# Optimization experiments

Measured on AMD Instinct MI355X. Metric: run time of the kernel, lower is better.

The kernel has to match this reference:

```python
import jax, jax.numpy as jnp
import numpy as np

N = 100000        # nodes
E = 1600000       # edges (avg degree 16)
D_NODE = 32
D_EDGE = 16
H = 64
C = 5


def setup_inputs() -> dict:
    key = jax.random.key(0)
    ks = jax.random.split(key, 11)
    x = jax.random.normal(ks[0], (N, D_NODE), jnp.float32)
    edge_index = jax.random.randint(ks[1], (2, E), 0, N, jnp.int32)
    edge_attr = jax.random.normal(ks[2], (E, D_EDGE), jnp.float32)
    W1 = jax.random.normal(ks[3], (D_NODE, H), jnp.float32) / np.sqrt(D_NODE)
    b1 = jax.random.normal(ks[4], (H,), jnp.float32) * 0.02
    W2 = jax.random.normal(ks[5], (H, H), jnp.float32) / np.sqrt(H)
    b2 = jax.random.normal(ks[6], (H,), jnp.float32) * 0.02
    Wc1 = jax.random.normal(ks[7], (2 * H + D_EDGE, 64), jnp.float32) / np.sqrt(2 * H + D_EDGE)
    bc1 = jax.random.normal(ks[8], (64,), jnp.float32) * 0.02
    Wc2 = jax.random.normal(ks[9], (64, C), jnp.float32) / np.sqrt(64)
    bc2 = jax.random.normal(ks[10], (C,), jnp.float32) * 0.02
    return {"x": x, "edge_index": edge_index, "edge_attr": edge_attr,
            "W1": W1, "b1": b1, "W2": W2, "b2": b2,
            "Wc1": Wc1, "bc1": bc1, "Wc2": Wc2, "bc2": bc2}


def gcn_conv(x, W, b, src, dst, n):
    h = x @ W                                   # [n, H]
    loop = jnp.arange(n, dtype=src.dtype)
    s = jnp.concatenate([src, loop])            # self-loops appended
    d = jnp.concatenate([dst, loop])
    deg = jax.ops.segment_sum(jnp.ones_like(s, h.dtype), d, num_segments=n)
    dinv = jax.lax.rsqrt(deg)                   # deg >= 1 due to self-loops
    norm = dinv[s] * dinv[d]                    # [E+n]
    out = jax.ops.segment_sum(h[s] * norm[:, None], d, num_segments=n)
    return out + b


def reference(x, edge_index, edge_attr, W1, b1, W2, b2, Wc1, bc1, Wc2, bc2):
    src, dst = edge_index[0], edge_index[1]
    n = x.shape[0]
    h = jax.nn.relu(gcn_conv(x, W1, b1, src, dst, n))
    h = gcn_conv(h, W2, b2, src, dst, n)
    # gather-concat edge features: [E, 2H + D_EDGE]
    ef = jnp.concatenate([h[src], h[dst], edge_attr], axis=1)
    out = jax.nn.relu(ef @ Wc1 + bc1) @ Wc2 + bc2
    return out
```

## Files before the change

kernel.cpp:

```cpp
#include <hip/hip_runtime.h>
#include <hip/hip_bf16.h>


typedef __attribute__((ext_vector_type(8))) short  bf16x8;
typedef __attribute__((ext_vector_type(16))) float f32x16;

__device__ inline short f2bf(float f)
{
    union { float f; unsigned u; } v; v.f = f;
    unsigned r = v.u + 0x7fff + ((v.u >> 16) & 1);
    return (short)(r >> 16);
}

__device__ inline float2 bfp2f(unsigned u)
{
    union { unsigned u; float f; } a, b;
    a.u = u << 16;
    b.u = u & 0xffff0000u;
    return make_float2(a.f, b.f);
}

__device__ inline unsigned packbf2(float a, float b)
{
    return (unsigned)(unsigned short)f2bf(a) | ((unsigned)(unsigned short)f2bf(b) << 16);
}

__global__ __launch_bounds__(256) void k_bcount(const int* __restrict__ ei, int* __restrict__ bcnt, int E)
{
    __shared__ int h[512];
    for (int i = threadIdx.x; i < 512; i += 256) h[i] = 0;
    __syncthreads();
    for (long e = (long)blockIdx.x * 256 + threadIdx.x; e < E; e += (long)gridDim.x * 256)
        atomicAdd(&h[ei[E + e] >> 8], 1);
    __syncthreads();
    for (int i = threadIdx.x; i < 512; i += 256)
        if (h[i]) atomicAdd(&bcnt[i], h[i]);
}

__global__ __launch_bounds__(512) void k_bscan(const int* __restrict__ bcnt, int nbk, int* __restrict__ bstart)
{
    __shared__ int s[512];
    int t = threadIdx.x;
    int v = (t < nbk) ? bcnt[t] : 0;
    s[t] = v;
    __syncthreads();
    for (int o = 1; o < 512; o <<= 1) {
        int a = (t >= o) ? s[t - o] : 0;
        __syncthreads();
        s[t] += a;
        __syncthreads();
    }
    if (t < nbk) bstart[t + 1] = s[t];
    if (t == 0) bstart[0] = 0;
}

__global__ __launch_bounds__(256) void k_binscatter(const int* __restrict__ ei, const int* __restrict__ bstart,
                                                    int* __restrict__ bcur, int2* __restrict__ ebs, int E)
{
    __shared__ int cnt[512], gb[512];
    const int tid = threadIdx.x;
    for (int i = tid; i < 512; i += 256) cnt[i] = 0;
    __syncthreads();
    const int base = blockIdx.x * 4096;
    int d[16], lp[16];
#pragma unroll
    for (int i = 0; i < 16; ++i) {
        int e = base + i * 256 + tid;
        if (e < E) {
            d[i] = ei[E + e];
            lp[i] = atomicAdd(&cnt[d[i] >> 8], 1);
        } else d[i] = -1;
    }
    __syncthreads();
    for (int i = tid; i < 512; i += 256) gb[i] = cnt[i] ? atomicAdd(&bcur[i], cnt[i]) : 0;
    __syncthreads();
#pragma unroll
    for (int i = 0; i < 16; ++i) {
        if (d[i] >= 0) {
            int e = base + i * 256 + tid;
            int b = d[i] >> 8;
            int2 p;
            p.x = ei[e];
            p.y = d[i];
            ebs[(size_t)bstart[b] + gb[b] + lp[i]] = p;
        }
    }
}

__global__ __launch_bounds__(256) void k_build(const int2* __restrict__ ebs, const int* __restrict__ bstart,
                                               int* __restrict__ rs, int* __restrict__ col,
                                               float* __restrict__ dinv,
                                               const float* __restrict__ x, unsigned short* __restrict__ xs,
                                               int N, int E)
{
    __shared__ int cnt[256], lstart[256], cnt2[256];
    const int b = blockIdx.x;
    const int base = b << 8;
    const int tid = threadIdx.x;
    cnt[tid] = 0; cnt2[tid] = 0;
    __syncthreads();
    const int s0 = bstart[b], s1 = bstart[b + 1];
    for (int i = s0 + tid; i < s1; i += 256) atomicAdd(&cnt[ebs[i].y - base], 1);
    __syncthreads();
    const int v = cnt[tid];
    lstart[tid] = v;
    __syncthreads();
    for (int o = 1; o < 256; o <<= 1) {
        int a = (tid >= o) ? lstart[tid - o] : 0;
        __syncthreads();
        lstart[tid] += a;
        __syncthreads();
    }
    const int node = base + tid;
    if (node < N) {
        rs[node] = s0 + lstart[tid] - v;
        dinv[node] = rsqrtf((float)(v + 1));
    }
    if (b == 0 && tid == 0) rs[N] = E;
    __syncthreads();
    for (int i = s0 + tid; i < s1; i += 256) {
        int2 p = ebs[i];
        int ln = p.y - base;
        int pos = atomicAdd(&cnt2[ln], 1);
        col[s0 + (lstart[ln] - cnt[ln]) + pos] = p.x;
    }
#pragma unroll
    for (int i = 0; i < 16; ++i) {
        int id = i * 256 + tid;
        int ni = id >> 4, pr = id & 15;
        int nd = base + ni;
        if (nd < N) {
            float dv = rsqrtf((float)(cnt[ni] + 1));
            float2 xv = *(const float2*)&x[(size_t)nd * 32 + pr * 2];
            *(unsigned*)(xs + (size_t)nd * 32 + pr * 2) = packbf2(xv.x * dv, xv.y * dv);
        }
    }
}

__global__ __launch_bounds__(256) void k_prep(const float* __restrict__ Wc1, const float* __restrict__ Wc2,
                                              const float* __restrict__ W2, const float* __restrict__ W1,
                                              short* __restrict__ Wc1T, short* __restrict__ Wc2T,
                                              short* __restrict__ W2T, short* __restrict__ W1T)
{
    int t = blockIdx.x * 256 + threadIdx.x;
    if (t < 9216) {
        int j = t / 144, k = t - j * 144;
        Wc1T[t] = f2bf(Wc1[k * 64 + j]);
    } else if (t < 11264) {
        int u = t - 9216;
        int rr = u / 64, p = u - rr * 64;
        int k = (p >> 1) + ((p & 1) << 5);
        Wc2T[u] = (rr < 5) ? f2bf(Wc2[k * 5 + rr]) : (short)0;
    } else if (t < 15360) {
        int u = t - 11264;
        int j = u / 64, k = u - j * 64;
        W2T[u] = f2bf(W2[k * 64 + j]);
    } else if (t < 17408) {
        int u = t - 15360;
        int j = u / 32, k = u - j * 32;
        W1T[u] = f2bf(W1[k * 64 + j]);
    }
}

__global__ __launch_bounds__(256) void k_agg_x(const unsigned short* __restrict__ xs,
                                               const float* __restrict__ dinv,
                                               const int* __restrict__ rs, const int* __restrict__ col,
                                               unsigned short* __restrict__ xagg, int n)
{
    const int tid = threadIdx.x;
    const int l   = tid & 7;
    const int v   = blockIdx.x * 32 + (tid >> 3);
    if (v >= n) return;

    uint2 sv = *(const uint2*)(xs + (size_t)v * 32 + l * 4);
    float2 aL = bfp2f(sv.x), aH = bfp2f(sv.y);
    int i = rs[v];
    const int end = rs[v + 1];
    for (; i + 8 <= end; i += 8) {
        int c0 = col[i],     c1 = col[i + 1], c2 = col[i + 2], c3 = col[i + 3];
        int c4 = col[i + 4], c5 = col[i + 5], c6 = col[i + 6], c7 = col[i + 7];
        uint2 u0 = *(const uint2*)(xs + (size_t)c0 * 32 + l * 4);
        uint2 u1 = *(const uint2*)(xs + (size_t)c1 * 32 + l * 4);
        uint2 u2 = *(const uint2*)(xs + (size_t)c2 * 32 + l * 4);
        uint2 u3 = *(const uint2*)(xs + (size_t)c3 * 32 + l * 4);
        uint2 u4 = *(const uint2*)(xs + (size_t)c4 * 32 + l * 4);
        uint2 u5 = *(const uint2*)(xs + (size_t)c5 * 32 + l * 4);
        uint2 u6 = *(const uint2*)(xs + (size_t)c6 * 32 + l * 4);
        uint2 u7 = *(const uint2*)(xs + (size_t)c7 * 32 + l * 4);
        float2 p;
        p = bfp2f(u0.x); aL.x += p.x; aL.y += p.y; p = bfp2f(u0.y); aH.x += p.x; aH.y += p.y;
        p = bfp2f(u1.x); aL.x += p.x; aL.y += p.y; p = bfp2f(u1.y); aH.x += p.x; aH.y += p.y;
        p = bfp2f(u2.x); aL.x += p.x; aL.y += p.y; p = bfp2f(u2.y); aH.x += p.x; aH.y += p.y;
        p = bfp2f(u3.x); aL.x += p.x; aL.y += p.y; p = bfp2f(u3.y); aH.x += p.x; aH.y += p.y;
        p = bfp2f(u4.x); aL.x += p.x; aL.y += p.y; p = bfp2f(u4.y); aH.x += p.x; aH.y += p.y;
        p = bfp2f(u5.x); aL.x += p.x; aL.y += p.y; p = bfp2f(u5.y); aH.x += p.x; aH.y += p.y;
        p = bfp2f(u6.x); aL.x += p.x; aL.y += p.y; p = bfp2f(u6.y); aH.x += p.x; aH.y += p.y;
        p = bfp2f(u7.x); aL.x += p.x; aL.y += p.y; p = bfp2f(u7.y); aH.x += p.x; aH.y += p.y;
    }
    for (; i < end; ++i) {
        uint2 u = *(const uint2*)(xs + (size_t)col[i] * 32 + l * 4);
        float2 p;
        p = bfp2f(u.x); aL.x += p.x; aL.y += p.y;
        p = bfp2f(u.y); aH.x += p.x; aH.y += p.y;
    }
    const float dv = dinv[v];
    uint2 o;
    o.x = packbf2(dv * aL.x, dv * aL.y);
    o.y = packbf2(dv * aH.x, dv * aH.y);
    *(uint2*)(xagg + (size_t)v * 32 + l * 4) = o;
}

__global__ __launch_bounds__(256) void k_agg64(const unsigned short* __restrict__ hsc,
                                               const float* __restrict__ dinv,
                                               const int* __restrict__ rs, const int* __restrict__ col,
                                               unsigned short* __restrict__ out, int n)
{
    const int tid = threadIdx.x;
    const int l   = tid & 15;
    const int v   = blockIdx.x * 16 + (tid >> 4);
    if (v >= n) return;

    uint2 sv = *(const uint2*)(hsc + (size_t)v * 64 + l * 4);
    float2 aL = bfp2f(sv.x), aH = bfp2f(sv.y);
    int i = rs[v];
    const int end = rs[v + 1];
    for (; i + 8 <= end; i += 8) {
        int c0 = col[i],     c1 = col[i + 1], c2 = col[i + 2], c3 = col[i + 3];
        int c4 = col[i + 4], c5 = col[i + 5], c6 = col[i + 6], c7 = col[i + 7];
        uint2 u0 = *(const uint2*)(hsc + (size_t)c0 * 64 + l * 4);
        uint2 u1 = *(const uint2*)(hsc + (size_t)c1 * 64 + l * 4);
        uint2 u2 = *(const uint2*)(hsc + (size_t)c2 * 64 + l * 4);
        uint2 u3 = *(const uint2*)(hsc + (size_t)c3 * 64 + l * 4);
        uint2 u4 = *(const uint2*)(hsc + (size_t)c4 * 64 + l * 4);
        uint2 u5 = *(const uint2*)(hsc + (size_t)c5 * 64 + l * 4);
        uint2 u6 = *(const uint2*)(hsc + (size_t)c6 * 64 + l * 4);
        uint2 u7 = *(const uint2*)(hsc + (size_t)c7 * 64 + l * 4);
        float2 p;
        p = bfp2f(u0.x); aL.x += p.x; aL.y += p.y; p = bfp2f(u0.y); aH.x += p.x; aH.y += p.y;
        p = bfp2f(u1.x); aL.x += p.x; aL.y += p.y; p = bfp2f(u1.y); aH.x += p.x; aH.y += p.y;
        p = bfp2f(u2.x); aL.x += p.x; aL.y += p.y; p = bfp2f(u2.y); aH.x += p.x; aH.y += p.y;
        p = bfp2f(u3.x); aL.x += p.x; aL.y += p.y; p = bfp2f(u3.y); aH.x += p.x; aH.y += p.y;
        p = bfp2f(u4.x); aL.x += p.x; aL.y += p.y; p = bfp2f(u4.y); aH.x += p.x; aH.y += p.y;
        p = bfp2f(u5.x); aL.x += p.x; aL.y += p.y; p = bfp2f(u5.y); aH.x += p.x; aH.y += p.y;
        p = bfp2f(u6.x); aL.x += p.x; aL.y += p.y; p = bfp2f(u6.y); aH.x += p.x; aH.y += p.y;
        p = bfp2f(u7.x); aL.x += p.x; aL.y += p.y; p = bfp2f(u7.y); aH.x += p.x; aH.y += p.y;
    }
    for (; i < end; ++i) {
        uint2 u = *(const uint2*)(hsc + (size_t)col[i] * 64 + l * 4);
        float2 p;
        p = bfp2f(u.x); aL.x += p.x; aL.y += p.y;
        p = bfp2f(u.y); aH.x += p.x; aH.y += p.y;
    }
    const float dv = dinv[v];
    uint2 o;
    o.x = packbf2(dv * aL.x, dv * aL.y);
    o.y = packbf2(dv * aH.x, dv * aH.y);
    *(uint2*)(out + (size_t)v * 64 + l * 4) = o;
}

__global__ __launch_bounds__(256) void k_node1(const unsigned short* __restrict__ xagg,
                                               const short* __restrict__ W1T,
                                               const float* __restrict__ b1, const float* __restrict__ dinv,
                                               unsigned short* __restrict__ h1s, int n)
{
    const int tid = threadIdx.x;
    const int w = tid >> 6, lane = tid & 63, r = lane & 31, kg = lane >> 5;
    const int nb = blockIdx.x * 128 + w * 32;

    bf16x8 a0[2], a1[2];
#pragma unroll
    for (int t = 0; t < 2; ++t) {
        a0[t] = *(const bf16x8*)&W1T[r * 32 + t * 16 + kg * 8];
        a1[t] = *(const bf16x8*)&W1T[(r + 32) * 32 + t * 16 + kg * 8];
    }

    int row = nb + r;
    if (row >= n) row = n - 1;
    f32x16 acc0 = {0.f}, acc1 = {0.f};
#pragma unroll
    for (int t = 0; t < 2; ++t) {
        bf16x8 b = *(const bf16x8*)&xagg[(size_t)row * 32 + t * 16 + kg * 8];
        acc0 = __builtin_amdgcn_mfma_f32_32x32x16_bf16(a0[t], b, acc0, 0, 0, 0);
        acc1 = __builtin_amdgcn_mfma_f32_32x32x16_bf16(a1[t], b, acc1, 0, 0, 0);
    }

    const int node = nb + r;
    if (node < n) {
        const float dv = dinv[node];
#pragma unroll
        for (int q = 0; q < 4; ++q) {
            const int j0 = 8 * q + 4 * kg;
            float4 bA = *(const float4*)&b1[j0];
            float4 bB = *(const float4*)&b1[j0 + 32];
            short4 s0, s1;
            float t0, t1;
            t0 = acc0[4 * q]     + bA.x; t0 = t0 > 0.f ? t0 : 0.f; s0.x = f2bf(t0 * dv);
            t0 = acc0[4 * q + 1] + bA.y; t0 = t0 > 0.f ? t0 : 0.f; s0.y = f2bf(t0 * dv);
            t0 = acc0[4 * q + 2] + bA.z; t0 = t0 > 0.f ? t0 : 0.f; s0.z = f2bf(t0 * dv);
            t0 = acc0[4 * q + 3] + bA.w; t0 = t0 > 0.f ? t0 : 0.f; s0.w = f2bf(t0 * dv);
            t1 = acc1[4 * q]     + bB.x; t1 = t1 > 0.f ? t1 : 0.f; s1.x = f2bf(t1 * dv);
            t1 = acc1[4 * q + 1] + bB.y; t1 = t1 > 0.f ? t1 : 0.f; s1.y = f2bf(t1 * dv);
            t1 = acc1[4 * q + 2] + bB.z; t1 = t1 > 0.f ? t1 : 0.f; s1.z = f2bf(t1 * dv);
            t1 = acc1[4 * q + 3] + bB.w; t1 = t1 > 0.f ? t1 : 0.f; s1.w = f2bf(t1 * dv);
            *(short4*)&h1s[(size_t)node * 64 + j0]      = s0;
            *(short4*)&h1s[(size_t)node * 64 + j0 + 32] = s1;
        }
    }
}

__global__ __launch_bounds__(256) void k_node2(const unsigned short* __restrict__ xagg2,
                                               const short* __restrict__ W2T,
                                               const float* __restrict__ b2,
                                               unsigned short* __restrict__ h2, int n)
{
    const int tid = threadIdx.x;
    const int w = tid >> 6, lane = tid & 63, r = lane & 31, kg = lane >> 5;
    const int nb = blockIdx.x * 128 + w * 32;

    bf16x8 a0[4], a1[4];
#pragma unroll
    for (int t = 0; t < 4; ++t) {
        a0[t] = *(const bf16x8*)&W2T[r * 64 + t * 16 + kg * 8];
        a1[t] = *(const bf16x8*)&W2T[(r + 32) * 64 + t * 16 + kg * 8];
    }

    int row = nb + r;
    if (row >= n) row = n - 1;
    f32x16 acc0 = {0.f}, acc1 = {0.f};
#pragma unroll
    for (int t = 0; t < 4; ++t) {
        bf16x8 b = *(const bf16x8*)&xagg2[(size_t)row * 64 + t * 16 + kg * 8];
        acc0 = __builtin_amdgcn_mfma_f32_32x32x16_bf16(a0[t], b, acc0, 0, 0, 0);
        acc1 = __builtin_amdgcn_mfma_f32_32x32x16_bf16(a1[t], b, acc1, 0, 0, 0);
    }

    const int node = nb + r;
    if (node < n) {
#pragma unroll
        for (int q = 0; q < 4; ++q) {
            const int j0 = 8 * q + 4 * kg;
            float4 bA = *(const float4*)&b2[j0];
            float4 bB = *(const float4*)&b2[j0 + 32];
            short4 s0, s1;
            s0.x = f2bf(acc0[4 * q]     + bA.x); s0.y = f2bf(acc0[4 * q + 1] + bA.y);
            s0.z = f2bf(acc0[4 * q + 2] + bA.z); s0.w = f2bf(acc0[4 * q + 3] + bA.w);
            s1.x = f2bf(acc1[4 * q]     + bB.x); s1.y = f2bf(acc1[4 * q + 1] + bB.y);
            s1.z = f2bf(acc1[4 * q + 2] + bB.z); s1.w = f2bf(acc1[4 * q + 3] + bB.w);
            *(short4*)&h2[(size_t)node * 64 + j0]      = s0;
            *(short4*)&h2[(size_t)node * 64 + j0 + 32] = s1;
        }
    }
}

__global__ __launch_bounds__(256) void k_edge_mlp_mfma(
    const unsigned short* __restrict__ h2bf, const float* __restrict__ eattr,
    const int* __restrict__ ei,
    const short* __restrict__ Wc1T, const float* __restrict__ bc1,
    const short* __restrict__ Wc2T, const float* __restrict__ bc2,
    float* __restrict__ out, int E)
{
    __shared__ char slab[4 * 8192];

    const int tid = threadIdx.x;
    const int w = tid >> 6, lane = tid & 63, r = lane & 31, kg = lane >> 5;
    const int q = lane & 3, sr = lane >> 2;

    char* myslab = slab + w * 8192;

    const long eb = (long)blockIdx.x * 128 + w * 32;
    long ecl = eb + r; if (ecl >= E) ecl = E - 1;
    const int ns = ei[ecl];
    const int nd = ei[E + ecl];

    bf16x8 aa;
    {
        const float* arow = &eattr[(size_t)ecl * 16];
        float4 alo = *(const float4*)&arow[kg * 8];
        float4 ahi = *(const float4*)&arow[kg * 8 + 4];
        aa[0] = f2bf(alo.x); aa[1] = f2bf(alo.y); aa[2] = f2bf(alo.z); aa[3] = f2bf(alo.w);
        aa[4] = f2bf(ahi.x); aa[5] = f2bf(ahi.y); aa[6] = f2bf(ahi.z); aa[7] = f2bf(ahi.w);
    }

    {
        int n0 = __shfl(ns, sr);
        int n1 = __shfl(ns, 16 + sr);
        int m0 = __shfl(nd, sr);
        int m1 = __shfl(nd, 16 + sr);
        int4 s0 = *(const int4*)&h2bf[(size_t)n0 * 64 + q * 8];
        int4 s1 = *(const int4*)&h2bf[(size_t)n0 * 64 + 32 + q * 8];
        int4 s2 = *(const int4*)&h2bf[(size_t)n1 * 64 + q * 8];
        int4 s3 = *(const int4*)&h2bf[(size_t)n1 * 64 + 32 + q * 8];
        int4 d0 = *(const int4*)&h2bf[(size_t)m0 * 64 + q * 8];
        int4 d1 = *(const int4*)&h2bf[(size_t)m0 * 64 + 32 + q * 8];
        int4 d2 = *(const int4*)&h2bf[(size_t)m1 * 64 + q * 8];
        int4 d3 = *(const int4*)&h2bf[(size_t)m1 * 64 + 32 + q * 8];
        const int x0 = (sr ^ q) * 16, x1 = (16 + (sr ^ q)) * 16;
        *(int4*)(myslab + q * 512 + x0)              = s0;
        *(int4*)(myslab + (4 + q) * 512 + x0)        = s1;
        *(int4*)(myslab + q * 512 + x1)              = s2;
        *(int4*)(myslab + (4 + q) * 512 + x1)        = s3;
        *(int4*)(myslab + 4096 + q * 512 + x0)       = d0;
        *(int4*)(myslab + 4096 + (4 + q) * 512 + x0) = d1;
        *(int4*)(myslab + 4096 + q * 512 + x1)       = d2;
        *(int4*)(myslab + 4096 + (4 + q) * 512 + x1) = d3;
    }

    f32x16 acc0, acc1;
    const float bias0 = bc1[r], bias1 = bc1[r + 32];
#pragma unroll
    for (int i = 0; i < 16; ++i) { acc0[i] = bias0; acc1[i] = bias1; }

#pragma unroll
    for (int t = 0; t < 4; ++t) {
        const int c = 2 * t + kg;
        bf16x8 a  = *(const bf16x8*)(myslab + c * 512 + ((r ^ (c & 3)) * 16));
        bf16x8 w0 = *(const bf16x8*)&Wc1T[r * 144 + t * 16 + kg * 8];
        bf16x8 w1 = *(const bf16x8*)&Wc1T[(r + 32) * 144 + t * 16 + kg * 8];
        acc0 = __builtin_amdgcn_mfma_f32_32x32x16_bf16(a, w0, acc0, 0, 0, 0);
        acc1 = __builtin_amdgcn_mfma_f32_32x32x16_bf16(a, w1, acc1, 0, 0, 0);
    }
#pragma unroll
    for (int t = 0; t < 4; ++t) {
        const int c = 2 * t + kg;
        bf16x8 a  = *(const bf16x8*)(myslab + 4096 + c * 512 + ((r ^ (c & 3)) * 16));
        bf16x8 w0 = *(const bf16x8*)&Wc1T[r * 144 + (4 + t) * 16 + kg * 8];
        bf16x8 w1 = *(const bf16x8*)&Wc1T[(r + 32) * 144 + (4 + t) * 16 + kg * 8];
        acc0 = __builtin_amdgcn_mfma_f32_32x32x16_bf16(a, w0, acc0, 0, 0, 0);
        acc1 = __builtin_amdgcn_mfma_f32_32x32x16_bf16(a, w1, acc1, 0, 0, 0);
    }
    {
        bf16x8 w0 = *(const bf16x8*)&Wc1T[r * 144 + 128 + kg * 8];
        bf16x8 w1 = *(const bf16x8*)&Wc1T[(r + 32) * 144 + 128 + kg * 8];
        acc0 = __builtin_amdgcn_mfma_f32_32x32x16_bf16(aa, w0, acc0, 0, 0, 0);
        acc1 = __builtin_amdgcn_mfma_f32_32x32x16_bf16(aa, w1, acc1, 0, 0, 0);
    }

#pragma unroll
    for (int reg = 0; reg < 16; ++reg) {
        const int row = (reg & 3) + 8 * (reg >> 2) + 4 * kg;
        float v0 = acc0[reg]; v0 = v0 > 0.f ? v0 : 0.f;
        float v1 = acc1[reg]; v1 = v1 > 0.f ? v1 : 0.f;
        *(unsigned*)(myslab + row * 128 + ((4 * r) ^ ((row & 7) << 4))) = packbf2(v0, v1);
    }

    const float bias2 = (r < 5) ? bc2[r] : 0.f;
    f32x16 acc2;
#pragma unroll
    for (int i = 0; i < 16; ++i) acc2[i] = bias2;
#pragma unroll
    for (int t2 = 0; t2 < 4; ++t2) {
        const int m = t2 * 2 + kg;
        bf16x8 a  = *(const bf16x8*)(myslab + r * 128 + ((16 * m) ^ ((r & 7) << 4)));
        bf16x8 bw = *(const bf16x8*)&Wc2T[r * 64 + t2 * 16 + kg * 8];
        acc2 = __builtin_amdgcn_mfma_f32_32x32x16_bf16(a, bw, acc2, 0, 0, 0);
    }

#pragma unroll
    for (int reg = 0; reg < 16; ++reg) {
        const int row = (reg & 3) + 8 * (reg >> 2) + 4 * kg;
        const long eo = eb + row;
        if (r < 5 && eo < E) out[(size_t)eo * 5 + r] = acc2[reg];
    }
}

extern "C" void kernel_launch(void* const* d_in, const int* in_sizes, int n_in,
                              void* d_out, int out_size, void* d_ws, size_t ws_size,
                              hipStream_t stream)
{
    const float* x     = (const float*)d_in[0];
    const int*   ei    = (const int*)d_in[1];
    const float* eattr = (const float*)d_in[2];
    const float* W1    = (const float*)d_in[3];
    const float* b1    = (const float*)d_in[4];
    const float* W2    = (const float*)d_in[5];
    const float* b2    = (const float*)d_in[6];
    const float* Wc1   = (const float*)d_in[7];
    const float* bc1   = (const float*)d_in[8];
    const float* Wc2   = (const float*)d_in[9];
    const float* bc2   = (const float*)d_in[10];
    float* outp = (float*)d_out;

    const int N = in_sizes[0] / 32;
    const int E = in_sizes[1] / 2;
    const int nbk = (N + 255) >> 8;

    size_t off = 0;
    char* base = (char*)d_ws;
    auto carve = [&](size_t bytes) -> void* {
        void* p = base + off;
        off += (bytes + 255) & ~(size_t)255;
        return p;
    };
    int*   bcnt   = (int*)carve(1024 * 4);
    int*   bcur   = bcnt + 512;
    int*   bstart = (int*)carve(520 * 4);
    float* dinv   = (float*)carve((size_t)N * 4);
    int*   rs     = (int*)carve((size_t)(N + 1) * 4);
    int*   col    = (int*)carve((size_t)E * 4);
    int2*  ebs    = (int2*)carve((size_t)E * 8);
    unsigned short* xs    = (unsigned short*)carve((size_t)N * 32 * 2);
    unsigned short* xagg  = (unsigned short*)carve((size_t)N * 32 * 2);
    unsigned short* h1s   = (unsigned short*)carve((size_t)N * 64 * 2);
    unsigned short* xagg2 = (unsigned short*)carve((size_t)N * 64 * 2);
    unsigned short* h2bf  = h1s;
    short* Wc1T   = (short*)carve(9216 * 2);
    short* Wc2T   = (short*)carve(2048 * 2);
    short* W2T    = (short*)carve(4096 * 2);
    short* W1T    = (short*)carve(2048 * 2);
    (void)n_in; (void)out_size; (void)ws_size;

    const int NAX = (N + 31) / 32;
    const int NA  = (N + 15) / 16;
    const int NM  = (N + 127) / 128;
    const int NT  = (E + 127) / 128;
    const int NSC = (E + 4095) / 4096;

    hipMemsetAsync(bcnt, 0, 1024 * 4, stream);

    k_prep<<<68, 256, 0, stream>>>(Wc1, Wc2, W2, W1, Wc1T, Wc2T, W2T, W1T);

    k_bcount<<<1024, 256, 0, stream>>>(ei, bcnt, E);
    k_bscan<<<1, 512, 0, stream>>>(bcnt, nbk, bstart);
    k_binscatter<<<NSC, 256, 0, stream>>>(ei, bstart, bcur, ebs, E);
    k_build<<<nbk, 256, 0, stream>>>(ebs, bstart, rs, col, dinv, x, xs, N, E);

    k_agg_x<<<NAX, 256, 0, stream>>>(xs, dinv, rs, col, xagg, N);
    k_node1<<<NM, 256, 0, stream>>>(xagg, W1T, b1, dinv, h1s, N);
    k_agg64<<<NA, 256, 0, stream>>>(h1s, dinv, rs, col, xagg2, N);
    k_node2<<<NM, 256, 0, stream>>>(xagg2, W2T, b2, h2bf, N);

    k_edge_mlp_mfma<<<NT, 256, 0, stream>>>(h2bf, eattr, ei, Wc1T, bc1, Wc2T, bc2, outp, E);
}
```

Baseline: 287.5 us.

## Fold W2 into edge MLP first-layer weights and pre-convert edge attributes to bf16

Because layer-2 GCN aggregation is linear, the W2 matmul is folded into the first edge-MLP weights: the source and destination blocks of Wc1 are premultiplied by W2, and b2 is folded into a new combined bias. This removes the k_node2 pass and its full-N read and write. Separately, when workspace allows, a new kernel converts edge_attr to bf16 before the edge MLP, which then reads half-width attributes. That conversion is an extra full pass over the edge attributes and may cost more traffic than it saves. Folding the weights in bf16 also changes rounding slightly.

```diff
diff --git a/kernel.cpp b/kernel.cpp
--- a/kernel.cpp
+++ b/kernel.cpp
@@ -139,27 +139,52 @@
 
 __global__ __launch_bounds__(256) void k_prep(const float* __restrict__ Wc1, const float* __restrict__ Wc2,
                                               const float* __restrict__ W2, const float* __restrict__ W1,
+                                              const float* __restrict__ bc1, const float* __restrict__ b2,
                                               short* __restrict__ Wc1T, short* __restrict__ Wc2T,
-                                              short* __restrict__ W2T, short* __restrict__ W1T)
+                                              short* __restrict__ W1T, float* __restrict__ bcp)
 {
     int t = blockIdx.x * 256 + threadIdx.x;
     if (t < 9216) {
-        int j = t / 144, k = t - j * 144;
-        Wc1T[t] = f2bf(Wc1[k * 64 + j]);
+        int j = t / 144, p = t - j * 144;
+        float val;
+        if (p < 64) {
+            float s = 0.f;
+            for (int k = 0; k < 64; ++k) s = fmaf(W2[p * 64 + k], Wc1[k * 64 + j], s);
+            val = s;
+        } else if (p < 128) {
+            int m = p - 64;
+            float s = 0.f;
+            for (int k = 0; k < 64; ++k) s = fmaf(W2[m * 64 + k], Wc1[(64 + k) * 64 + j], s);
+            val = s;
+        } else {
+            val = Wc1[p * 64 + j];
+        }
+        Wc1T[t] = f2bf(val);
     } else if (t < 11264) {
         int u = t - 9216;
         int rr = u / 64, p = u - rr * 64;
         int k = (p >> 1) + ((p & 1) << 5);
         Wc2T[u] = (rr < 5) ? f2bf(Wc2[k * 5 + rr]) : (short)0;
-    } else if (t < 15360) {
+    } else if (t < 13312) {
         int u = t - 11264;
-        int j = u / 64, k = u - j * 64;
-        W2T[u] = f2bf(W2[k * 64 + j]);
-    } else if (t < 17408) {
-        int u = t - 15360;
         int j = u / 32, k = u - j * 32;
         W1T[u] = f2bf(W1[k * 64 + j]);
-    }
+    } else if (t < 13376) {
+        int j = t - 13312;
+        float s = bc1[j];
+        for (int k = 0; k < 64; ++k) s = fmaf(b2[k], Wc1[k * 64 + j] + Wc1[(64 + k) * 64 + j], s);
+        bcp[j] = s;
+    }
+}
+
+__global__ __launch_bounds__(256) void k_ea(const float* __restrict__ ea, unsigned short* __restrict__ eabf, long n4)
+{
+    long id = (long)blockIdx.x * 256 + threadIdx.x;
+    if (id >= n4) return;
+    float4 v = *(const float4*)&ea[id * 4];
+    short4 o;
+    o.x = f2bf(v.x); o.y = f2bf(v.y); o.z = f2bf(v.z); o.w = f2bf(v.w);
+    *(short4*)&eabf[id * 4] = o;
 }
 
 __global__ __launch_bounds__(256) void k_agg_x(const unsigned short* __restrict__ xs,
@@ -308,54 +333,11 @@
     }
 }
 
-__global__ __launch_bounds__(256) void k_node2(const unsigned short* __restrict__ xagg2,
-                                               const short* __restrict__ W2T,
-                                               const float* __restrict__ b2,
-                                               unsigned short* __restrict__ h2, int n)
-{
-    const int tid = threadIdx.x;
-    const int w = tid >> 6, lane = tid & 63, r = lane & 31, kg = lane >> 5;
-    const int nb = blockIdx.x * 128 + w * 32;
-
-    bf16x8 a0[4], a1[4];
-#pragma unroll
-    for (int t = 0; t < 4; ++t) {
-        a0[t] = *(const bf16x8*)&W2T[r * 64 + t * 16 + kg * 8];
-        a1[t] = *(const bf16x8*)&W2T[(r + 32) * 64 + t * 16 + kg * 8];
-    }
-
-    int row = nb + r;
-    if (row >= n) row = n - 1;
-    f32x16 acc0 = {0.f}, acc1 = {0.f};
-#pragma unroll
-    for (int t = 0; t < 4; ++t) {
-        bf16x8 b = *(const bf16x8*)&xagg2[(size_t)row * 64 + t * 16 + kg * 8];
-        acc0 = __builtin_amdgcn_mfma_f32_32x32x16_bf16(a0[t], b, acc0, 0, 0, 0);
-        acc1 = __builtin_amdgcn_mfma_f32_32x32x16_bf16(a1[t], b, acc1, 0, 0, 0);
-    }
-
-    const int node = nb + r;
-    if (node < n) {
-#pragma unroll
-        for (int q = 0; q < 4; ++q) {
-            const int j0 = 8 * q + 4 * kg;
-            float4 bA = *(const float4*)&b2[j0];
-            float4 bB = *(const float4*)&b2[j0 + 32];
-            short4 s0, s1;
-            s0.x = f2bf(acc0[4 * q]     + bA.x); s0.y = f2bf(acc0[4 * q + 1] + bA.y);
-            s0.z = f2bf(acc0[4 * q + 2] + bA.z); s0.w = f2bf(acc0[4 * q + 3] + bA.w);
-            s1.x = f2bf(acc1[4 * q]     + bB.x); s1.y = f2bf(acc1[4 * q + 1] + bB.y);
-            s1.z = f2bf(acc1[4 * q + 2] + bB.z); s1.w = f2bf(acc1[4 * q + 3] + bB.w);
-            *(short4*)&h2[(size_t)node * 64 + j0]      = s0;
-            *(short4*)&h2[(size_t)node * 64 + j0 + 32] = s1;
-        }
-    }
-}
-
+template <int ABF>
 __global__ __launch_bounds__(256) void k_edge_mlp_mfma(
-    const unsigned short* __restrict__ h2bf, const float* __restrict__ eattr,
+    const unsigned short* __restrict__ zrow, const void* __restrict__ eattr,
     const int* __restrict__ ei,
-    const short* __restrict__ Wc1T, const float* __restrict__ bc1,
+    const short* __restrict__ Wc1T, const float* __restrict__ bcp,
     const short* __restrict__ Wc2T, const float* __restrict__ bc2,
     float* __restrict__ out, int E)
 {
@@ -373,8 +355,10 @@
     const int nd = ei[E + ecl];
 
     bf16x8 aa;
-    {
-        const float* arow = &eattr[(size_t)ecl * 16];
+    if (ABF) {
+        aa = *(const bf16x8*)((const unsigned short*)eattr + (size_t)ecl * 16 + kg * 8);
+    } else {
+        const float* arow = (const float*)eattr + (size_t)ecl * 16;
         float4 alo = *(const float4*)&arow[kg * 8];
         float4 ahi = *(const float4*)&arow[kg * 8 + 4];
         aa[0] = f2bf(alo.x); aa[1] = f2bf(alo.y); aa[2] = f2bf(alo.z); aa[3] = f2bf(alo.w);
@@ -386,14 +370,14 @@
         int n1 = __shfl(ns, 16 + sr);
         int m0 = __shfl(nd, sr);
         int m1 = __shfl(nd, 16 + sr);
-        int4 s0 = *(const int4*)&h2bf[(size_t)n0 * 64 + q * 8];
-        int4 s1 = *(const int4*)&h2bf[(size_t)n0 * 64 + 32 + q * 8];
-        int4 s2 = *(const int4*)&h2bf[(size_t)n1 * 64 + q * 8];
-        int4 s3 = *(const int4*)&h2bf[(size_t)n1 * 64 + 32 + q * 8];
-        int4 d0 = *(const int4*)&h2bf[(size_t)m0 * 64 + q * 8];
-        int4 d1 = *(const int4*)&h2bf[(size_t)m0 * 64 + 32 + q * 8];
-        int4 d2 = *(const int4*)&h2bf[(size_t)m1 * 64 + q * 8];
-        int4 d3 = *(const int4*)&h2bf[(size_t)m1 * 64 + 32 + q * 8];
+        int4 s0 = *(const int4*)&zrow[(size_t)n0 * 64 + q * 8];
+        int4 s1 = *(const int4*)&zrow[(size_t)n0 * 64 + 32 + q * 8];
+        int4 s2 = *(const int4*)&zrow[(size_t)n1 * 64 + q * 8];
+        int4 s3 = *(const int4*)&zrow[(size_t)n1 * 64 + 32 + q * 8];
+        int4 d0 = *(const int4*)&zrow[(size_t)m0 * 64 + q * 8];
+        int4 d1 = *(const int4*)&zrow[(size_t)m0 * 64 + 32 + q * 8];
+        int4 d2 = *(const int4*)&zrow[(size_t)m1 * 64 + q * 8];
+        int4 d3 = *(const int4*)&zrow[(size_t)m1 * 64 + 32 + q * 8];
         const int x0 = (sr ^ q) * 16, x1 = (16 + (sr ^ q)) * 16;
         *(int4*)(myslab + q * 512 + x0)              = s0;
         *(int4*)(myslab + (4 + q) * 512 + x0)        = s1;
@@ -406,7 +390,7 @@
     }
 
     f32x16 acc0, acc1;
-    const float bias0 = bc1[r], bias1 = bc1[r + 32];
+    const float bias0 = bcp[r], bias1 = bcp[r + 32];
 #pragma unroll
     for (int i = 0; i < 16; ++i) { acc0[i] = bias0; acc1[i] = bias1; }
 
@@ -502,12 +486,13 @@
     unsigned short* xagg  = (unsigned short*)carve((size_t)N * 32 * 2);
     unsigned short* h1s   = (unsigned short*)carve((size_t)N * 64 * 2);
     unsigned short* xagg2 = (unsigned short*)carve((size_t)N * 64 * 2);
-    unsigned short* h2bf  = h1s;
     short* Wc1T   = (short*)carve(9216 * 2);
     short* Wc2T   = (short*)carve(2048 * 2);
-    short* W2T    = (short*)carve(4096 * 2);
     short* W1T    = (short*)carve(2048 * 2);
-    (void)n_in; (void)out_size; (void)ws_size;
+    float* bcp    = (float*)carve(64 * 4);
+    unsigned short* eabf = (unsigned short*)carve((size_t)E * 16 * 2);
+    const bool use_abf = (off <= ws_size);
+    (void)n_in; (void)out_size;
 
     const int NAX = (N + 31) / 32;
     const int NA  = (N + 15) / 16;
@@ -517,7 +502,8 @@
 
     hipMemsetAsync(bcnt, 0, 1024 * 4, stream);
 
-    k_prep<<<68, 256, 0, stream>>>(Wc1, Wc2, W2, W1, Wc1T, Wc2T, W2T, W1T);
+    k_prep<<<68, 256, 0, stream>>>(Wc1, Wc2, W2, W1, bc1, b2, Wc1T, Wc2T, W1T, bcp);
+    if (use_abf) k_ea<<<(int)(((long)E * 4 + 255) / 256), 256, 0, stream>>>(eattr, eabf, (long)E * 4);
 
     k_bcount<<<1024, 256, 0, stream>>>(ei, bcnt, E);
     k_bscan<<<1, 512, 0, stream>>>(bcnt, nbk, bstart);
@@ -527,7 +513,9 @@
     k_agg_x<<<NAX, 256, 0, stream>>>(xs, dinv, rs, col, xagg, N);
     k_node1<<<NM, 256, 0, stream>>>(xagg, W1T, b1, dinv, h1s, N);
     k_agg64<<<NA, 256, 0, stream>>>(h1s, dinv, rs, col, xagg2, N);
-    k_node2<<<NM, 256, 0, stream>>>(xagg2, W2T, b2, h2bf, N);
-
-    k_edge_mlp_mfma<<<NT, 256, 0, stream>>>(h2bf, eattr, ei, Wc1T, bc1, Wc2T, bc2, outp, E);
-}
+
+    if (use_abf)
+        k_edge_mlp_mfma<1><<<NT, 256, 0, stream>>>(xagg2, eabf, ei, Wc1T, bcp, Wc2T, bc2, outp, E);
+    else
+        k_edge_mlp_mfma<0><<<NT, 256, 0, stream>>>(xagg2, eattr, ei, Wc1T, bcp, Wc2T, bc2, outp, E);
+}
```

New measurement: 293.9 us. +2.2%, slower.
